# Kernel optimization log

Hardware: AMD Instinct MI355X
Metric: run time of the kernel (lower is better)

The kernel has to match this reference:

```python
import jax, jax.numpy as jnp
import numpy as np

B, N, F_IN, F_OUT = 8, 2048, 128, 64
ALPHA = 0.2  # LeakyReLU negative slope
NEG_INF = -9e15


def setup_inputs() -> dict:
    key = jax.random.key(0)
    k1, k2, k3, k4 = jax.random.split(key, 4)
    h = jax.random.normal(k1, (B, N, F_IN), dtype=jnp.float32)
    adj = jax.random.randint(k2, (B, N, N), 0, 2, dtype=jnp.int32)
    # xavier_uniform with gain=1.414 approximated by scaled normals (values are arbitrary params)
    W = jax.random.normal(k3, (F_IN, F_OUT), dtype=jnp.float32) * (1.414 * np.sqrt(2.0 / (F_IN + F_OUT)))
    a = jax.random.normal(k4, (2 * F_OUT, 1), dtype=jnp.float32) * (1.414 * np.sqrt(2.0 / (2 * F_OUT + 1)))
    return {"h": h, "adj": adj, "W": W, "a": a}


def reference(h, adj, W, a):
    # Wh: [B, N, F_out]
    Wh = jnp.einsum('bnf,fo->bno', h, W)
    Fo = W.shape[1]
    a1 = a[:Fo, 0]   # [F_out]
    a2 = a[Fo:, 0]   # [F_out]
    # e[b,i,j] = leakyrelu(Wh[b,i]@a1 + Wh[b,j]@a2)  (== cat(Wh_i,Wh_j)@a, same math, no N^2*2F blowup)
    e1 = jnp.einsum('bno,o->bn', Wh, a1)  # [B, N]
    e2 = jnp.einsum('bno,o->bn', Wh, a2)  # [B, N]
    e = e1[:, :, None] + e2[:, None, :]   # [B, N, N]
    e = jnp.where(e > 0, e, ALPHA * e)    # LeakyReLU
    e = jnp.where(adj > 0, e, NEG_INF)    # mask non-edges
    attention = jax.nn.softmax(e, axis=-1)
    # dropout is identity in inference mode (deterministic reference)
    h_prime = jnp.einsum('bij,bjo->bio', attention, Wh)  # [B, N, F_out]
    return jax.nn.elu(h_prime)  # concat=True branch
```

## Files before the change

### kernel.cpp

```cpp
#include <hip/hip_runtime.h>
#include <hip/hip_bf16.h>

#define BB 8
#define NN 2048
#define FIN 128
#define FO 64
#define ALPHA 0.2f

typedef __attribute__((ext_vector_type(8))) short bf16x8;
typedef __attribute__((ext_vector_type(4))) float f32x4;
typedef __attribute__((ext_vector_type(4))) int i32x4;

typedef __attribute__((address_space(1))) const void gvoid;
typedef __attribute__((address_space(3))) void lvoid;

__device__ inline void gl_lds16(const void* g, void* l) {
    __builtin_amdgcn_global_load_lds((gvoid*)g, (lvoid*)l, 16, 0, 0);
}

__device__ inline short f2bf(float x) {
    unsigned u = __float_as_uint(x);
    u += 0x7fffu + ((u >> 16) & 1u);
    return (short)(u >> 16);
}

__global__ __launch_bounds__(256) void wh_kernel(
    const float* __restrict__ h, const float* __restrict__ W,
    const float* __restrict__ a, float* __restrict__ e1, float* __restrict__ e2,
    short* __restrict__ whF)
{
    __shared__ float hs[32][FIN];
    const int r0 = blockIdx.x * 32;
    const int t = threadIdx.x;
    const float4* hsrc = (const float4*)(h + (size_t)r0 * FIN);
    float4* hdst = (float4*)(&hs[0][0]);
#pragma unroll
    for (int k = 0; k < 4; k++) hdst[t + 256 * k] = hsrc[t + 256 * k];
    __syncthreads();

    const int o = t & 63;
    const int wv = t >> 6;
    float acc[8];
#pragma unroll
    for (int rr = 0; rr < 8; rr++) acc[rr] = 0.f;

    for (int f = 0; f < FIN; f += 4) {
        const float w0 = W[(f + 0) * FO + o];
        const float w1 = W[(f + 1) * FO + o];
        const float w2 = W[(f + 2) * FO + o];
        const float w3 = W[(f + 3) * FO + o];
#pragma unroll
        for (int rr = 0; rr < 8; rr++) {
            float4 hv = *(const float4*)&hs[wv * 8 + rr][f];
            acc[rr] = fmaf(hv.x, w0, acc[rr]);
            acc[rr] = fmaf(hv.y, w1, acc[rr]);
            acc[rr] = fmaf(hv.z, w2, acc[rr]);
            acc[rr] = fmaf(hv.w, w3, acc[rr]);
        }
    }

    const int b   = r0 / NN;
    const int ib0 = r0 - b * NN;
    const int ibb = ib0 + wv * 8;
    const int jc  = ibb >> 5;
    const int qq  = (ibb >> 3) & 3;
    const int ot  = o >> 4, mm = o & 15;
    const int L   = mm + qq * 16;
    bf16x8 frag;
#pragma unroll
    for (int rr = 0; rr < 8; rr++) frag[rr] = f2bf(acc[rr]);
    *(bf16x8*)(whF + ((((size_t)(b * 64 + jc) * 4 + ot) * 64 + L) * 8)) = frag;

    const float a1 = a[o], a2 = a[FO + o];
#pragma unroll
    for (int rr = 0; rr < 8; rr++) {
        float v1 = acc[rr] * a1, v2 = acc[rr] * a2;
#pragma unroll
        for (int msk = 32; msk >= 1; msk >>= 1) {
            v1 += __shfl_xor(v1, msk, 64);
            v2 += __shfl_xor(v2, msk, 64);
        }
        if (o == 0) { e1[r0 + wv * 8 + rr] = v1; e2[r0 + wv * 8 + rr] = v2; }
    }
}

__global__ __launch_bounds__(256) void e2max_kernel(
    const float* __restrict__ e2, float* __restrict__ e2max)
{
    const int b = blockIdx.x;
    const int t = threadIdx.x;
    float m = -1e30f;
    for (int j = t; j < NN; j += 256) m = fmaxf(m, e2[b * NN + j]);
#pragma unroll
    for (int k = 32; k >= 1; k >>= 1) m = fmaxf(m, __shfl_xor(m, k, 64));
    __shared__ float red[4];
    if ((t & 63) == 0) red[t >> 6] = m;
    __syncthreads();
    if (t == 0) e2max[b] = fmaxf(fmaxf(red[0], red[1]), fmaxf(red[2], red[3]));
}

struct SMemS {
    int   adjs[4][4][2][16][8][4];
    float e2s[4][512];
};
struct SMemC { float comb[4][2][16][64]; float lsum[4][2][16]; };
union SMemU { SMemS s; SMemC c; };

struct WFrag { bf16x8 f0, f1, f2, f3; };

#define CFENCE asm volatile("" ::: "memory")
#define WAITVM_(n) asm volatile("s_waitcnt vmcnt(" #n ")" ::: "memory")
#define WAITVM(n) WAITVM_(n)

#define STAGE(k) do { \
    const int bf_ = (k) & 3; \
    gl_lds16(asrc0 + (size_t)(k) * 32, &ladj[bf_][0][0][0][0]); \
    gl_lds16(asrc1 + (size_t)(k) * 32, &ladj[bf_][0][8][0][0]); \
    gl_lds16(asrc2 + (size_t)(k) * 32, &ladj[bf_][1][0][0][0]); \
    gl_lds16(asrc3 + (size_t)(k) * 32, &ladj[bf_][1][8][0][0]); \
    CFENCE; \
} while (0)

#define WLOAD(dst, k) do { \
    const short* bfp = whFw + (size_t)(k) * 2048; \
    dst.f0 = *(const bf16x8*)(bfp); \
    dst.f1 = *(const bf16x8*)(bfp + 512); \
    dst.f2 = *(const bf16x8*)(bfp + 1024); \
    dst.f3 = *(const bf16x8*)(bfp + 1536); \
    CFENCE; \
} while (0)

#define SCORE8(AU, VA0, VA1, E1C, NMB) do { \
    float pe[8]; \
    _Pragma("unroll") \
    for (int jj = 0; jj < 8; jj++) { \
        const int   av = (jj < 4) ? VA0[jj] : VA1[jj - 4]; \
        const float ej = (jj < 4) ? ev0[jj] : ev1[jj - 4]; \
        const float s  = fmaf(ej, L2E, E1C); \
        const float lk = fmaxf(s, ALPHA * s); \
        pe[jj] = __builtin_amdgcn_exp2f(lk + fmaf((float)av, 4000.0f, NMB)); \
    } \
    _Pragma("unroll") \
    for (int jj = 0; jj < 4; jj++) \
        AU.u[jj] = __builtin_amdgcn_perm(__float_as_uint(pe[2 * jj + 1]), \
                                         __float_as_uint(pe[2 * jj]), 0x07060302u); \
} while (0)

#define STEPC(k, VM, WF) do { \
    WAITVM(VM); \
    const int bf_ = (k) & 3; \
    i32x4 va00 = *(const i32x4*)&ladj[bf_][0][m][u0][0]; \
    i32x4 va01 = *(const i32x4*)&ladj[bf_][0][m][u1][0]; \
    i32x4 va10 = *(const i32x4*)&ladj[bf_][1][m][u0][0]; \
    i32x4 va11 = *(const i32x4*)&ladj[bf_][1][m][u1][0]; \
    f32x4 ev0 = *(const f32x4*)&le2[(k) * 32 + q * 8]; \
    f32x4 ev1 = *(const f32x4*)&le2[(k) * 32 + q * 8 + 4]; \
    union { unsigned u[4]; bf16x8 v; } au0, au1; \
    SCORE8(au0, va00, va01, E1v0, negMiB0); \
    SCORE8(au1, va10, va11, E1v1, negMiB1); \
    acc00 = __builtin_amdgcn_mfma_f32_16x16x32_bf16(au0.v, WF.f0, acc00, 0, 0, 0); \
    acc01 = __builtin_amdgcn_mfma_f32_16x16x32_bf16(au0.v, WF.f1, acc01, 0, 0, 0); \
    acc02 = __builtin_amdgcn_mfma_f32_16x16x32_bf16(au0.v, WF.f2, acc02, 0, 0, 0); \
    acc03 = __builtin_amdgcn_mfma_f32_16x16x32_bf16(au0.v, WF.f3, acc03, 0, 0, 0); \
    acc04 = __builtin_amdgcn_mfma_f32_16x16x32_bf16(au0.v, ones, acc04, 0, 0, 0); \
    acc10 = __builtin_amdgcn_mfma_f32_16x16x32_bf16(au1.v, WF.f0, acc10, 0, 0, 0); \
    acc11 = __builtin_amdgcn_mfma_f32_16x16x32_bf16(au1.v, WF.f1, acc11, 0, 0, 0); \
    acc12 = __builtin_amdgcn_mfma_f32_16x16x32_bf16(au1.v, WF.f2, acc12, 0, 0, 0); \
    acc13 = __builtin_amdgcn_mfma_f32_16x16x32_bf16(au1.v, WF.f3, acc13, 0, 0, 0); \
    acc14 = __builtin_amdgcn_mfma_f32_16x16x32_bf16(au1.v, ones, acc14, 0, 0, 0); \
} while (0)

__global__ __launch_bounds__(256) void attn_kernel(
    const int* __restrict__ adj, const float* __restrict__ e1,
    const float* __restrict__ e2, const float* __restrict__ e2max,
    const short* __restrict__ whF, float* __restrict__ out)
{
    __shared__ __align__(16) SMemU sm;
    const int t = threadIdx.x, w = t >> 6, lane = t & 63;
    const int m = lane & 15, q = lane >> 4;
    const int blk = blockIdx.x;
    const int b = blk >> 6, i0 = (blk & 63) * 32;

    const float L2E = 1.4426950408889634f;
    const float e2m = e2max[b];
    const float e1v0 = e1[b * NN + i0 + m];
    const float e1v1 = e1[b * NN + i0 + 16 + m];
    float mr0 = e1v0 + e2m; mr0 = mr0 > 0.f ? mr0 : ALPHA * mr0;
    float mr1 = e1v1 + e2m; mr1 = mr1 > 0.f ? mr1 : ALPHA * mr1;
    const float E1v0 = e1v0 * L2E, E1v1 = e1v1 * L2E;
    const float negMiB0 = -(mr0 * L2E + 4000.0f);
    const float negMiB1 = -(mr1 * L2E + 4000.0f);

    const int l8 = lane >> 3, c7 = lane & 7;
    const int csw = (c7 ^ l8) * 4;
    const int* asrc0 = adj + ((size_t)(b * NN + i0 + l8)) * NN + w * 512 + csw;
    const int* asrc1 = asrc0 + (size_t)8 * NN;
    const int* asrc2 = asrc0 + (size_t)16 * NN;
    const int* asrc3 = asrc0 + (size_t)24 * NN;
    int (*ladj)[2][16][8][4] = sm.s.adjs[w];
    float* le2 = sm.s.e2s[w];
    const float* e2src = e2 + b * NN + w * 512 + lane * 4;

    const short* whFw = whF + (size_t)b * (64 * 4 * 64 * 8)
                            + (size_t)(w * 16) * 2048 + lane * 8;

    f32x4 z = {0.f,0.f,0.f,0.f};
    f32x4 acc00 = z, acc01 = z, acc02 = z, acc03 = z, acc04 = z;
    f32x4 acc10 = z, acc11 = z, acc12 = z, acc13 = z, acc14 = z;
    bf16x8 ones;
#pragma unroll
    for (int jj = 0; jj < 8; jj++) ones[jj] = (short)0x3F80;

    const int u0 = (q * 2) ^ (m & 7);
    const int u1 = u0 ^ 1;

    gl_lds16(e2src,       &le2[0]);
    gl_lds16(e2src + 256, &le2[256]);
    CFENCE;
    STAGE(0); STAGE(1); STAGE(2);
    WFrag W0f, W1f;
    WLOAD(W0f, 0); WLOAD(W1f, 1);

#pragma unroll 1
    for (int k = 0; k < 12; k += 2) {
        WFrag Wa; WLOAD(Wa, k + 2); STAGE(k + 3); STEPC(k, 20, W0f); W0f = Wa;
        WFrag Wb; WLOAD(Wb, k + 3); STAGE(k + 4); STEPC(k + 1, 20, W1f); W1f = Wb;
    }
    { WFrag Wa; WLOAD(Wa, 14); STAGE(15); STEPC(12, 20, W0f); W0f = Wa; }
    { WFrag Wb; WLOAD(Wb, 15);            STEPC(13, 20, W1f); W1f = Wb; }
    STEPC(14, 12, W0f);
    STEPC(15,  4, W1f);

    __syncthreads();
    if (m == 0) {
#pragma unroll
        for (int r = 0; r < 4; r++) {
            sm.c.lsum[w][0][q * 4 + r] = acc04[r];
            sm.c.lsum[w][1][q * 4 + r] = acc14[r];
        }
    }
#pragma unroll
    for (int ot = 0; ot < 4; ot++) {
        f32x4 a0 = (ot == 0) ? acc00 : (ot == 1) ? acc01 : (ot == 2) ? acc02 : acc03;
        f32x4 a1 = (ot == 0) ? acc10 : (ot == 1) ? acc11 : (ot == 2) ? acc12 : acc13;
#pragma unroll
        for (int reg = 0; reg < 4; reg++) {
            sm.c.comb[w][0][q * 4 + reg][ot * 16 + m] = a0[reg];
            sm.c.comb[w][1][q * 4 + reg][ot * 16 + m] = a1[reg];
        }
    }
    __syncthreads();

#pragma unroll
    for (int it = 0; it < 2; it++) {
        const int idx = t + it * 256;
        const int row = idx >> 4;
        const int tl = row >> 4, r16 = row & 15;
        const int c0 = (idx & 15) * 4;
        f32x4 sum = *(const f32x4*)&sm.c.comb[0][tl][r16][c0];
#pragma unroll
        for (int ww = 1; ww < 4; ww++) {
            f32x4 sv = *(const f32x4*)&sm.c.comb[ww][tl][r16][c0];
            sum.x += sv.x; sum.y += sv.y; sum.z += sv.z; sum.w += sv.w;
        }
        float l = sm.c.lsum[0][tl][r16] + sm.c.lsum[1][tl][r16]
                + sm.c.lsum[2][tl][r16] + sm.c.lsum[3][tl][r16];
        l = fmaxf(l, 1e-30f);
        const float rl = 1.f / l;
        f32x4 res;
        float vr[4] = { sum.x * rl, sum.y * rl, sum.z * rl, sum.w * rl };
#pragma unroll
        for (int kk = 0; kk < 4; kk++)
            res[kk] = vr[kk] > 0.f ? vr[kk] : (__expf(vr[kk]) - 1.f);
        *(f32x4*)&out[((size_t)(b * NN + i0 + row)) * FO + c0] = res;
    }
}

extern "C" void kernel_launch(void* const* d_in, const int* in_sizes, int n_in,
                              void* d_out, int out_size, void* d_ws, size_t ws_size,
                              hipStream_t stream) {
    const float* h   = (const float*)d_in[0];
    const int*   adj = (const int*)d_in[1];
    const float* W   = (const float*)d_in[2];
    const float* a   = (const float*)d_in[3];
    float* out = (float*)d_out;

    char* ws = (char*)d_ws;
    short* whF = (short*)ws;
    size_t off = (size_t)BB * 64 * 4 * 64 * 8 * sizeof(short);
    float* e1  = (float*)(ws + off);  off += (size_t)BB * NN * 4;
    float* e2  = (float*)(ws + off);  off += (size_t)BB * NN * 4;
    float* e2m = (float*)(ws + off);

    wh_kernel<<<(BB * NN) / 32, 256, 0, stream>>>(h, W, a, e1, e2, whF);
    e2max_kernel<<<BB, 256, 0, stream>>>(e2, e2m);
    attn_kernel<<<BB * (NN / 32), 256, 0, stream>>>(adj, e1, e2, e2m, whF, out);
}
```

Before: 219.3 us.

## Pre-pack adjacency into bitmasks in a separate kernel before attention

Adds a pack kernel that reads the int32 adjacency matrix with coalesced loads and turns it into 64-bit ballot bitmasks. The attention kernel then loads the small packed mask for its 32 rows into shared memory once. It drops the multi-buffered global-to-LDS adjacency staging pipeline and pulls each score's mask bit with shifts. The goal is to take the large adjacency stream out of the compute-heavy kernel, which has few blocks, and give it to a highly parallel bandwidth kernel. The cost is an extra launch and a small write and re-read of the packed masks.

```diff
diff --git a/kernel.cpp b/kernel.cpp
--- a/kernel.cpp
+++ b/kernel.cpp
@@ -99,27 +99,28 @@
     if (t == 0) e2max[b] = fmaxf(fmaxf(red[0], red[1]), fmaxf(red[2], red[3]));
 }
 
-struct SMemS {
-    int   adjs[4][4][2][16][8][4];
-    float e2s[4][512];
-};
+__global__ __launch_bounds__(256) void pack_kernel(
+    const int* __restrict__ adj, unsigned long long* __restrict__ pk)
+{
+    const int t = threadIdx.x, wv = t >> 6, lane = t & 63;
+    const size_t row0 = (size_t)blockIdx.x * 8;
+#pragma unroll
+    for (int rr = 0; rr < 8; rr++) {
+        const size_t row = row0 + rr;
+        const int* src = adj + row * NN + wv * 512;
+#pragma unroll
+        for (int c = 0; c < 8; c++) {
+            unsigned long long mk = __ballot(src[c * 64 + lane] > 0);
+            if (lane == 0) pk[row * 32 + wv * 8 + c] = mk;
+        }
+    }
+}
+
+struct SMemS { unsigned pk[32][68]; float e2s[4][512]; };
 struct SMemC { float comb[4][2][16][64]; float lsum[4][2][16]; };
 union SMemU { SMemS s; SMemC c; };
 
 struct WFrag { bf16x8 f0, f1, f2, f3; };
-
-#define CFENCE asm volatile("" ::: "memory")
-#define WAITVM_(n) asm volatile("s_waitcnt vmcnt(" #n ")" ::: "memory")
-#define WAITVM(n) WAITVM_(n)
-
-#define STAGE(k) do { \
-    const int bf_ = (k) & 3; \
-    gl_lds16(asrc0 + (size_t)(k) * 32, &ladj[bf_][0][0][0][0]); \
-    gl_lds16(asrc1 + (size_t)(k) * 32, &ladj[bf_][0][8][0][0]); \
-    gl_lds16(asrc2 + (size_t)(k) * 32, &ladj[bf_][1][0][0][0]); \
-    gl_lds16(asrc3 + (size_t)(k) * 32, &ladj[bf_][1][8][0][0]); \
-    CFENCE; \
-} while (0)
 
 #define WLOAD(dst, k) do { \
     const short* bfp = whFw + (size_t)(k) * 2048; \
@@ -127,18 +128,17 @@
     dst.f1 = *(const bf16x8*)(bfp + 512); \
     dst.f2 = *(const bf16x8*)(bfp + 1024); \
     dst.f3 = *(const bf16x8*)(bfp + 1536); \
-    CFENCE; \
 } while (0)
 
-#define SCORE8(AU, VA0, VA1, E1C, NMB) do { \
+#define SCORE8(AU, D, E1C, NM2) do { \
     float pe[8]; \
     _Pragma("unroll") \
     for (int jj = 0; jj < 8; jj++) { \
-        const int   av = (jj < 4) ? VA0[jj] : VA1[jj - 4]; \
+        const float fb = (float)((D >> (q8 + jj)) & 1u); \
         const float ej = (jj < 4) ? ev0[jj] : ev1[jj - 4]; \
         const float s  = fmaf(ej, L2E, E1C); \
         const float lk = fmaxf(s, ALPHA * s); \
-        pe[jj] = __builtin_amdgcn_exp2f(lk + fmaf((float)av, 4000.0f, NMB)); \
+        pe[jj] = __builtin_amdgcn_exp2f(lk + fmaf(fb, 16000.f, NM2)); \
     } \
     _Pragma("unroll") \
     for (int jj = 0; jj < 4; jj++) \
@@ -146,18 +146,14 @@
                                          __float_as_uint(pe[2 * jj]), 0x07060302u); \
 } while (0)
 
-#define STEPC(k, VM, WF) do { \
-    WAITVM(VM); \
-    const int bf_ = (k) & 3; \
-    i32x4 va00 = *(const i32x4*)&ladj[bf_][0][m][u0][0]; \
-    i32x4 va01 = *(const i32x4*)&ladj[bf_][0][m][u1][0]; \
-    i32x4 va10 = *(const i32x4*)&ladj[bf_][1][m][u0][0]; \
-    i32x4 va11 = *(const i32x4*)&ladj[bf_][1][m][u1][0]; \
+#define STEPC(k, WF) do { \
+    const unsigned d0 = lspk[m][w16 + (k)]; \
+    const unsigned d1 = lspk[16 + m][w16 + (k)]; \
     f32x4 ev0 = *(const f32x4*)&le2[(k) * 32 + q * 8]; \
     f32x4 ev1 = *(const f32x4*)&le2[(k) * 32 + q * 8 + 4]; \
     union { unsigned u[4]; bf16x8 v; } au0, au1; \
-    SCORE8(au0, va00, va01, E1v0, negMiB0); \
-    SCORE8(au1, va10, va11, E1v1, negMiB1); \
+    SCORE8(au0, d0, E1v0, negMi20); \
+    SCORE8(au1, d1, E1v1, negMi21); \
     acc00 = __builtin_amdgcn_mfma_f32_16x16x32_bf16(au0.v, WF.f0, acc00, 0, 0, 0); \
     acc01 = __builtin_amdgcn_mfma_f32_16x16x32_bf16(au0.v, WF.f1, acc01, 0, 0, 0); \
     acc02 = __builtin_amdgcn_mfma_f32_16x16x32_bf16(au0.v, WF.f2, acc02, 0, 0, 0); \
@@ -171,13 +167,14 @@
 } while (0)
 
 __global__ __launch_bounds__(256) void attn_kernel(
-    const int* __restrict__ adj, const float* __restrict__ e1,
+    const unsigned long long* __restrict__ pkg, const float* __restrict__ e1,
     const float* __restrict__ e2, const float* __restrict__ e2max,
     const short* __restrict__ whF, float* __restrict__ out)
 {
     __shared__ __align__(16) SMemU sm;
     const int t = threadIdx.x, w = t >> 6, lane = t & 63;
     const int m = lane & 15, q = lane >> 4;
+    const int q8 = q * 8, w16 = w * 16;
     const int blk = blockIdx.x;
     const int b = blk >> 6, i0 = (blk & 63) * 32;
 
@@ -188,19 +185,24 @@
     float mr0 = e1v0 + e2m; mr0 = mr0 > 0.f ? mr0 : ALPHA * mr0;
     float mr1 = e1v1 + e2m; mr1 = mr1 > 0.f ? mr1 : ALPHA * mr1;
     const float E1v0 = e1v0 * L2E, E1v1 = e1v1 * L2E;
-    const float negMiB0 = -(mr0 * L2E + 4000.0f);
-    const float negMiB1 = -(mr1 * L2E + 4000.0f);
-
-    const int l8 = lane >> 3, c7 = lane & 7;
-    const int csw = (c7 ^ l8) * 4;
-    const int* asrc0 = adj + ((size_t)(b * NN + i0 + l8)) * NN + w * 512 + csw;
-    const int* asrc1 = asrc0 + (size_t)8 * NN;
-    const int* asrc2 = asrc0 + (size_t)16 * NN;
-    const int* asrc3 = asrc0 + (size_t)24 * NN;
-    int (*ladj)[2][16][8][4] = sm.s.adjs[w];
+    const float negMi20 = -(mr0 * L2E) - 16000.0f;
+    const float negMi21 = -(mr1 * L2E) - 16000.0f;
+
+    {
+        const unsigned* pg = (const unsigned*)pkg + (size_t)(b * NN + i0) * 64;
+        const int r = t >> 3, c = (t & 7) * 8;
+        i32x4 v0 = *(const i32x4*)(pg + r * 64 + c);
+        i32x4 v1 = *(const i32x4*)(pg + r * 64 + c + 4);
+        *(i32x4*)&sm.s.pk[r][c] = v0;
+        *(i32x4*)&sm.s.pk[r][c + 4] = v1;
+    }
     float* le2 = sm.s.e2s[w];
     const float* e2src = e2 + b * NN + w * 512 + lane * 4;
-
+    gl_lds16(e2src,       &le2[0]);
+    gl_lds16(e2src + 256, &le2[256]);
+    __syncthreads();
+
+    const unsigned (*lspk)[68] = sm.s.pk;
     const short* whFw = whF + (size_t)b * (64 * 4 * 64 * 8)
                             + (size_t)(w * 16) * 2048 + lane * 8;
 
@@ -211,25 +213,17 @@
 #pragma unroll
     for (int jj = 0; jj < 8; jj++) ones[jj] = (short)0x3F80;
 
-    const int u0 = (q * 2) ^ (m & 7);
-    const int u1 = u0 ^ 1;
-
-    gl_lds16(e2src,       &le2[0]);
-    gl_lds16(e2src + 256, &le2[256]);
-    CFENCE;
-    STAGE(0); STAGE(1); STAGE(2);
     WFrag W0f, W1f;
     WLOAD(W0f, 0); WLOAD(W1f, 1);
-
 #pragma unroll 1
     for (int k = 0; k < 12; k += 2) {
-        WFrag Wa; WLOAD(Wa, k + 2); STAGE(k + 3); STEPC(k, 20, W0f); W0f = Wa;
-        WFrag Wb; WLOAD(Wb, k + 3); STAGE(k + 4); STEPC(k + 1, 20, W1f); W1f = Wb;
-    }
-    { WFrag Wa; WLOAD(Wa, 14); STAGE(15); STEPC(12, 20, W0f); W0f = Wa; }
-    { WFrag Wb; WLOAD(Wb, 15);            STEPC(13, 20, W1f); W1f = Wb; }
-    STEPC(14, 12, W0f);
-    STEPC(15,  4, W1f);
+        WFrag Wa; WLOAD(Wa, k + 2); STEPC(k, W0f); W0f = Wa;
+        WFrag Wb; WLOAD(Wb, k + 3); STEPC(k + 1, W1f); W1f = Wb;
+    }
+    { WFrag Wa; WLOAD(Wa, 14); STEPC(12, W0f); W0f = Wa; }
+    { WFrag Wb; WLOAD(Wb, 15); STEPC(13, W1f); W1f = Wb; }
+    STEPC(14, W0f);
+    STEPC(15, W1f);
 
     __syncthreads();
     if (m == 0) {
@@ -290,9 +284,11 @@
     size_t off = (size_t)BB * 64 * 4 * 64 * 8 * sizeof(short);
     float* e1  = (float*)(ws + off);  off += (size_t)BB * NN * 4;
     float* e2  = (float*)(ws + off);  off += (size_t)BB * NN * 4;
-    float* e2m = (float*)(ws + off);
+    float* e2m = (float*)(ws + off);  off += 256;
+    unsigned long long* pk = (unsigned long long*)(ws + off);
 
     wh_kernel<<<(BB * NN) / 32, 256, 0, stream>>>(h, W, a, e1, e2, whF);
     e2max_kernel<<<BB, 256, 0, stream>>>(e2, e2m);
-    attn_kernel<<<BB * (NN / 32), 256, 0, stream>>>(adj, e1, e2, e2m, whF, out);
-}
+    pack_kernel<<<(BB * NN) / 8, 256, 0, stream>>>(adj, pk);
+    attn_kernel<<<BB * (NN / 32), 256, 0, stream>>>(pk, e1, e2, e2m, whF, out);
+}
```

New measurement: 247.8 us. 13.0% more time.
